# Optimization experiments

Hardware: AMD Instinct MI355X
Metric: run time of the kernel (lower is better)

## Reference

```python
import jax, jax.numpy as jnp
import numpy as np

B, S, D, H, E, K = 4, 2048, 1024, 2048, 8, 2


def setup_inputs() -> dict:
    key = jax.random.key(0)
    ks = jax.random.split(key, 5)
    x = jax.random.normal(ks[0], (B, S, D), dtype=jnp.float32)
    Wr = jax.random.normal(ks[1], (D, E), dtype=jnp.float32) * 0.02  # router weight
    w1 = jax.random.normal(ks[2], (E, D, H), dtype=jnp.float32) * 0.02  # gate proj per expert
    w3 = jax.random.normal(ks[3], (E, D, H), dtype=jnp.float32) * 0.02  # up proj per expert
    w2 = jax.random.normal(ks[4], (E, H, D), dtype=jnp.float32) * 0.02  # down proj per expert
    return {"x": x, "Wr": Wr, "w1": w1, "w2": w2, "w3": w3}


def reference(x, Wr, w1, w2, w3):
    b, s, d = x.shape
    e = Wr.shape[1]
    flat = x.reshape(b * s, d)                      # [T, D]
    logits = flat @ Wr                              # [T, E]
    probs = jax.nn.softmax(logits, axis=-1)
    vals, idx = jax.lax.top_k(probs, K)             # [T, K]
    weights = vals / jnp.sum(vals, axis=-1, keepdims=True)
    onehot = jax.nn.one_hot(idx, e, dtype=flat.dtype)   # [T, K, E]
    cw = jnp.einsum('tke,tk->te', onehot, weights)      # combine weight per (token, expert)

    # naive dense: every expert computes every token, masked by combine weights
    out = jnp.zeros_like(flat)
    for ei in range(e):  # fixed small structural loop over experts
        h = jax.nn.silu(flat @ w1[ei]) * (flat @ w3[ei])   # [T, H]
        out = out + (h @ w2[ei]) * cw[:, ei:ei + 1]

    # aux load-balancing loss (usage uses any() over top-k slots, as in torch code)
    usage = (onehot.sum(axis=1) > 0).astype(flat.dtype).mean(axis=0)  # [E]
    prob_mass = probs.mean(axis=0)                                     # [E]
    aux_loss = e * jnp.sum(usage * prob_mass)
    return out.reshape(b, s, d), aux_loss
```

## Files before the change

kernel.cpp:

```cpp
#include <hip/hip_runtime.h>
#include <hip/hip_bf16.h>
#include <cstdint>
#include <cstddef>

#define T_TOK 8192
#define DIM   1024
#define HID   2048
#define NE    8
#define CAP   2816

typedef __attribute__((ext_vector_type(8))) short bf16x8;
typedef __attribute__((ext_vector_type(4))) float f32x4;
using bf16 = __hip_bfloat16;

__device__ __forceinline__ void gload16(const bf16* g, bf16* l) {
    __builtin_amdgcn_global_load_lds(
        (const __attribute__((address_space(1))) unsigned int*)(g),
        (__attribute__((address_space(3))) unsigned int*)(l), 16, 0, 0);
}
__device__ __forceinline__ float b2f(unsigned short u) {
    return __uint_as_float(((unsigned int)u) << 16);
}
#define MFMA16(a, b, c) __builtin_amdgcn_mfma_f32_16x16x32_bf16((a), (b), (c), 0, 0, 0)
#define BARRIER() asm volatile("s_barrier" ::: "memory")
#define WAITVM6() asm volatile("s_waitcnt vmcnt(6)" ::: "memory")
#define WAITVM4() asm volatile("s_waitcnt vmcnt(4)" ::: "memory")
#define WAITVM0() asm volatile("s_waitcnt vmcnt(0)" ::: "memory")

__global__ __launch_bounds__(256) void k_transpose_all(const float* __restrict__ w1,
                                                       const float* __restrict__ w3,
                                                       const float* __restrict__ w2,
                                                       bf16* __restrict__ w1t,
                                                       bf16* __restrict__ w3t,
                                                       bf16* __restrict__ w2t) {
    __shared__ float tile[64][65];
    int z = blockIdx.z;
    const float* in = (z == 0) ? w1 : (z == 1) ? w3 : w2;
    bf16* out = (z == 0) ? w1t : (z == 1) ? w3t : w2t;
    int R = (z == 2) ? HID : DIM;
    int C = (z == 2) ? DIM : HID;
    int e = blockIdx.y;
    int ct = C >> 6;
    int r0 = (blockIdx.x / ct) << 6;
    int c0 = (blockIdx.x % ct) << 6;
    const float* src = in + (size_t)e * R * C;
    bf16* dst = out + (size_t)e * R * C;
    int s = threadIdx.x & 15, g = threadIdx.x >> 4;
#pragma unroll
    for (int j = 0; j < 4; ++j) {
        int row = j * 16 + g;
        float4 v = *(const float4*)(src + (size_t)(r0 + row) * C + c0 + s * 4);
        tile[row][s * 4 + 0] = v.x; tile[row][s * 4 + 1] = v.y;
        tile[row][s * 4 + 2] = v.z; tile[row][s * 4 + 3] = v.w;
    }
    __syncthreads();
#pragma unroll
    for (int j = 0; j < 4; ++j) {
        int c = j * 16 + g;
        int r = s * 4;
        bf16 o[4] = {__float2bfloat16(tile[r][c]),     __float2bfloat16(tile[r + 1][c]),
                     __float2bfloat16(tile[r + 2][c]), __float2bfloat16(tile[r + 3][c])};
        *(uint2*)(dst + (size_t)(c0 + c) * R + r0 + r) = *(const uint2*)o;
    }
}

__global__ __launch_bounds__(256) void k_logits(const float* __restrict__ x,
                                                const float* __restrict__ Wr,
                                                float* __restrict__ logits,
                                                bf16* __restrict__ xb) {
    __shared__ float wl[NE][DIM];
    for (int o = threadIdx.x; o < NE * DIM; o += 256) {
        int e = o >> 10, d = o & (DIM - 1);
        wl[e][d] = Wr[d * NE + e];
    }
    __syncthreads();
    int wid = threadIdx.x >> 6, lane = threadIdx.x & 63;
    int t = blockIdx.x * 4 + wid;
    const float* xr = x + (size_t)t * DIM;
    double acc[NE];
#pragma unroll
    for (int e = 0; e < NE; ++e) acc[e] = 0.0;
#pragma unroll
    for (int i = 0; i < DIM / 256; ++i) {
        int base = i * 256 + lane * 4;
        float4 v = *(const float4*)(xr + base);
        bf16 o[4] = {__float2bfloat16(v.x), __float2bfloat16(v.y),
                     __float2bfloat16(v.z), __float2bfloat16(v.w)};
        *(uint2*)(xb + (size_t)t * DIM + base) = *(const uint2*)o;
#pragma unroll
        for (int e = 0; e < NE; ++e)
            acc[e] += (double)v.x * wl[e][base] + (double)v.y * wl[e][base + 1]
                    + (double)v.z * wl[e][base + 2] + (double)v.w * wl[e][base + 3];
    }
#pragma unroll
    for (int e = 0; e < NE; ++e) {
        double v = acc[e];
        for (int m = 32; m >= 1; m >>= 1) v += __shfl_xor(v, m);
        if (lane == 0) logits[t * NE + e] = (float)v;
    }
}

__global__ __launch_bounds__(256) void k_route(const float* __restrict__ logits,
                                               int* counts, int* seg_tok, float* seg_w,
                                               int* slotpos, float* probsum) {
    int t = blockIdx.x * 256 + threadIdx.x;
    float l[NE];
#pragma unroll
    for (int e = 0; e < NE; ++e) l[e] = logits[t * NE + e];
    float mx = l[0];
#pragma unroll
    for (int e = 1; e < NE; ++e) mx = fmaxf(mx, l[e]);
    float p[NE], s = 0.f;
#pragma unroll
    for (int e = 0; e < NE; ++e) { p[e] = expf(l[e] - mx); s += p[e]; }
    float inv = 1.f / s;
#pragma unroll
    for (int e = 0; e < NE; ++e) p[e] *= inv;
    int e0 = 0; float v0 = p[0];
#pragma unroll
    for (int e = 1; e < NE; ++e) if (p[e] > v0) { v0 = p[e]; e0 = e; }
    int e1 = -1; float v1 = -1.f;
#pragma unroll
    for (int e = 0; e < NE; ++e) if (e != e0 && p[e] > v1) { v1 = p[e]; e1 = e; }
    float wsum = v0 + v1;
    float w0 = v0 / wsum, w1 = v1 / wsum;

    int lane = threadIdx.x & 63, wid = threadIdx.x >> 6;
    __shared__ float ps[4][NE];
#pragma unroll
    for (int e = 0; e < NE; ++e) {
        float v = p[e];
        for (int m = 32; m >= 1; m >>= 1) v += __shfl_xor(v, m);
        if (lane == 0) ps[wid][e] = v;
    }
    __syncthreads();
    if (threadIdx.x < NE) {
        float v = ps[0][threadIdx.x] + ps[1][threadIdx.x] + ps[2][threadIdx.x] + ps[3][threadIdx.x];
        atomicAdd(&probsum[threadIdx.x], v);
    }
    for (int slot = 0; slot < 2; ++slot) {
        int   e  = slot ? e1 : e0;
        float wv = slot ? w1 : w0;
#pragma unroll
        for (int ex = 0; ex < NE; ++ex) {
            unsigned long long m = __ballot(e == ex);
            if (e == ex) {
                int leader = __ffsll(m) - 1;
                int base = 0;
                if (lane == leader) base = atomicAdd(&counts[ex], __popcll(m));
                base = __shfl(base, leader);
                int pos = base + (int)__popcll(m & ((1ull << lane) - 1ull));
                if (pos < CAP) {
                    seg_tok[ex * CAP + pos] = t;
                    seg_w[ex * CAP + pos]  = wv;
                    slotpos[2 * t + slot]  = ex * CAP + pos;
                } else {
                    slotpos[2 * t + slot]  = -1;
                }
            }
        }
    }
}

__global__ __launch_bounds__(512, 2) void k_gemm1(const bf16* __restrict__ xb,
                                                  const bf16* __restrict__ w1t,
                                                  const bf16* __restrict__ w3t,
                                                  const int* __restrict__ counts,
                                                  const int* __restrict__ seg_tok,
                                                  bf16* __restrict__ h) {
    __shared__ __align__(16) bf16 lds[65536];
    __shared__ int toks[256];
    const int NTL = HID / 128;
    int flat = blockIdx.y * gridDim.x + blockIdx.x;
    int cpx  = (gridDim.x * NE) >> 3;
    int swz  = (flat & 7) * cpx + (flat >> 3);
    int e    = swz / gridDim.x;
    int tile = swz % gridDim.x;
    int mtile = tile / NTL, ntile = tile % NTL;
    int cnt = counts[e]; if (cnt > CAP) cnt = CAP;
    if (mtile * 256 >= cnt) return;

    int tx = threadIdx.x, lane = tx & 63, wid = tx >> 6;
    for (int i = tx; i < 256; i += 512) {
        int slot = mtile * 256 + i;
        toks[i] = seg_tok[e * CAP + (slot < cnt ? slot : 0)];
    }
    __syncthreads();

    int sr  = tx >> 2;
    int sc8 = (((tx & 3) ^ ((tx >> 3) & 3)) << 3);
    const bf16* sApLo = xb + (size_t)toks[sr]       * DIM + sc8;
    const bf16* sApHi = xb + (size_t)toks[128 + sr] * DIM + sc8;
    const bf16* sBg   = w1t + ((size_t)e * HID + ntile * 128 + sr) * DIM + sc8;
    const bf16* sBu   = w3t + ((size_t)e * HID + ntile * 128 + sr) * DIM + sc8;
    bf16* dA = lds + tx * 8;
    bf16* dB = lds + 32768 + tx * 8;

    int l15 = lane & 15, lh = lane >> 4;
    int wm = wid >> 2, wn = wid & 3;
    int ach = ((lh ^ ((l15 >> 1) & 3)) << 3);
    const bf16* rA = lds + (wm * 128 + l15) * 32 + ach;
    const bf16* rB = lds + 32768 + (wn * 32 + l15) * 32 + ach;

    f32x4 accg[8][2], accu[8][2];
    f32x4 zero4 = {0.f, 0.f, 0.f, 0.f};
#pragma unroll
    for (int m = 0; m < 8; ++m)
#pragma unroll
        for (int n = 0; n < 2; ++n) { accg[m][n] = zero4; accu[m][n] = zero4; }

#define STAGE_A1(s, ko) do { \
        gload16(sApLo + (ko), dA + (s) * 8192); \
        gload16(sApHi + (ko), dA + (s) * 8192 + 4096); } while (0)
#define STAGE_B1(s, ko) do { \
        gload16(sBg + (ko), dB + (s) * 8192); \
        gload16(sBu + (ko), dB + (s) * 8192 + 4096); } while (0)

    STAGE_A1(0, 0);  STAGE_B1(0, 0);
    STAGE_A1(1, 32); STAGE_B1(1, 32);

    const int NT = DIM / 32;
    bf16x8 g0, g1, u0, u1;
#pragma unroll 1
    for (int k = 0; k < NT; ++k) {
        int cs = (k & 3) * 8192, ps = (k + 2) & 3;
        bool st = (k + 2 < NT);
        int ko = (k + 2) * 32;
        if (st) STAGE_A1(ps, ko);
        if (k < NT - 2) WAITVM6(); else if (k < NT - 1) WAITVM4(); else WAITVM0();
        BARRIER();
        {
            const bf16* Ab = rA + cs;
            bf16x8 a0 = *(const bf16x8*)(Ab);
            bf16x8 a1 = *(const bf16x8*)(Ab + 512);
            bf16x8 a2 = *(const bf16x8*)(Ab + 1024);
            bf16x8 a3 = *(const bf16x8*)(Ab + 1536);
            const bf16* Bb = rB + cs;
            g0 = *(const bf16x8*)(Bb);
            g1 = *(const bf16x8*)(Bb + 512);
            u0 = *(const bf16x8*)(Bb + 4096);
            u1 = *(const bf16x8*)(Bb + 4608);
            __builtin_amdgcn_s_setprio(1);
            accg[0][0] = MFMA16(a0, g0, accg[0][0]); accg[1][0] = MFMA16(a1, g0, accg[1][0]);
            accg[2][0] = MFMA16(a2, g0, accg[2][0]); accg[3][0] = MFMA16(a3, g0, accg[3][0]);
            accg[0][1] = MFMA16(a0, g1, accg[0][1]); accg[1][1] = MFMA16(a1, g1, accg[1][1]);
            accg[2][1] = MFMA16(a2, g1, accg[2][1]); accg[3][1] = MFMA16(a3, g1, accg[3][1]);
            accu[0][0] = MFMA16(a0, u0, accu[0][0]); accu[1][0] = MFMA16(a1, u0, accu[1][0]);
            accu[2][0] = MFMA16(a2, u0, accu[2][0]); accu[3][0] = MFMA16(a3, u0, accu[3][0]);
            accu[0][1] = MFMA16(a0, u1, accu[0][1]); accu[1][1] = MFMA16(a1, u1, accu[1][1]);
            accu[2][1] = MFMA16(a2, u1, accu[2][1]); accu[3][1] = MFMA16(a3, u1, accu[3][1]);
            __builtin_amdgcn_s_setprio(0);
        }
        if (st) STAGE_B1(ps, ko);
        BARRIER();
        {
            const bf16* Ab = rA + cs + 2048;
            bf16x8 a4 = *(const bf16x8*)(Ab);
            bf16x8 a5 = *(const bf16x8*)(Ab + 512);
            bf16x8 a6 = *(const bf16x8*)(Ab + 1024);
            bf16x8 a7 = *(const bf16x8*)(Ab + 1536);
            __builtin_amdgcn_s_setprio(1);
            accg[4][0] = MFMA16(a4, g0, accg[4][0]); accg[5][0] = MFMA16(a5, g0, accg[5][0]);
            accg[6][0] = MFMA16(a6, g0, accg[6][0]); accg[7][0] = MFMA16(a7, g0, accg[7][0]);
            accg[4][1] = MFMA16(a4, g1, accg[4][1]); accg[5][1] = MFMA16(a5, g1, accg[5][1]);
            accg[6][1] = MFMA16(a6, g1, accg[6][1]); accg[7][1] = MFMA16(a7, g1, accg[7][1]);
            accu[4][0] = MFMA16(a4, u0, accu[4][0]); accu[5][0] = MFMA16(a5, u0, accu[5][0]);
            accu[6][0] = MFMA16(a6, u0, accu[6][0]); accu[7][0] = MFMA16(a7, u0, accu[7][0]);
            accu[4][1] = MFMA16(a4, u1, accu[4][1]); accu[5][1] = MFMA16(a5, u1, accu[5][1]);
            accu[6][1] = MFMA16(a6, u1, accu[6][1]); accu[7][1] = MFMA16(a7, u1, accu[7][1]);
            __builtin_amdgcn_s_setprio(0);
        }
    }
#undef STAGE_A1
#undef STAGE_B1

    bf16* hdst = h + ((size_t)e * CAP + (size_t)mtile * 256) * HID + ntile * 128;
#pragma unroll
    for (int m = 0; m < 8; ++m)
#pragma unroll
        for (int n = 0; n < 2; ++n)
#pragma unroll
            for (int r = 0; r < 4; ++r) {
                int row = wm * 128 + m * 16 + lh * 4 + r;
                int col = wn * 32 + n * 16 + l15;
                float gg = accg[m][n][r], uu = accu[m][n][r];
                float hv = gg / (1.f + __expf(-gg)) * uu;
                hdst[(size_t)row * HID + col] = __float2bfloat16(hv);
            }
}

__global__ __launch_bounds__(512, 2) void k_gemm2(const bf16* __restrict__ h,
                                                  const bf16* __restrict__ w2t,
                                                  const int* __restrict__ counts,
                                                  const float* __restrict__ seg_w,
                                                  bf16* __restrict__ ybuf) {
    __shared__ __align__(16) bf16 lds[65536];
    __shared__ float wts[256];
    const int NTL = DIM / 256;
    int flat = blockIdx.y * gridDim.x + blockIdx.x;
    int cpx  = (gridDim.x * NE) >> 3;
    int swz  = (flat & 7) * cpx + (flat >> 3);
    int e    = swz / gridDim.x;
    int tile = swz % gridDim.x;
    int mtile = tile / NTL, ntile = tile % NTL;
    int cnt = counts[e]; if (cnt > CAP) cnt = CAP;
    if (mtile * 256 >= cnt) return;

    int tx = threadIdx.x, lane = tx & 63, wid = tx >> 6;
    for (int i = tx; i < 256; i += 512) {
        int slot = mtile * 256 + i;
        wts[i] = (slot < cnt) ? seg_w[e * CAP + slot] : 0.f;
    }
    __syncthreads();

    int sr  = tx >> 2;
    int sc8 = (((tx & 3) ^ ((tx >> 3) & 3)) << 3);
    const bf16* sApLo = h + ((size_t)e * CAP + mtile * 256 + sr) * HID + sc8;
    const bf16* sApHi = h + ((size_t)e * CAP + mtile * 256 + 128 + sr) * HID + sc8;
    const bf16* sBpLo = w2t + ((size_t)e * DIM + ntile * 256 + sr) * HID + sc8;
    const bf16* sBpHi = w2t + ((size_t)e * DIM + ntile * 256 + 128 + sr) * HID + sc8;
    bf16* dA = lds + tx * 8;
    bf16* dB = lds + 32768 + tx * 8;

    int l15 = lane & 15, lh = lane >> 4;
    int wm = wid >> 2, wn = wid & 3;
    int ach = ((lh ^ ((l15 >> 1) & 3)) << 3);
    const bf16* rA = lds + (wm * 128 + l15) * 32 + ach;
    const bf16* rB = lds + 32768 + (wn * 64 + l15) * 32 + ach;

    f32x4 acc[8][4];
    f32x4 zero4 = {0.f, 0.f, 0.f, 0.f};
#pragma unroll
    for (int m = 0; m < 8; ++m)
#pragma unroll
        for (int n = 0; n < 4; ++n) acc[m][n] = zero4;

#define STAGE_A2(s, ko) do { \
        gload16(sApLo + (ko), dA + (s) * 8192); \
        gload16(sApHi + (ko), dA + (s) * 8192 + 4096); } while (0)
#define STAGE_B2(s, ko) do { \
        gload16(sBpLo + (ko), dB + (s) * 8192); \
        gload16(sBpHi + (ko), dB + (s) * 8192 + 4096); } while (0)

    STAGE_A2(0, 0);  STAGE_B2(0, 0);
    STAGE_A2(1, 32); STAGE_B2(1, 32);

    const int NT = HID / 32;
    bf16x8 b0, b1, b2, b3;
#pragma unroll 1
    for (int k = 0; k < NT; ++k) {
        int cs = (k & 3) * 8192, ps = (k + 2) & 3;
        bool st = (k + 2 < NT);
        int ko = (k + 2) * 32;
        if (st) STAGE_A2(ps, ko);
        if (k < NT - 2) WAITVM6(); else if (k < NT - 1) WAITVM4(); else WAITVM0();
        BARRIER();
        {
            const bf16* Ab = rA + cs;
            bf16x8 a0 = *(const bf16x8*)(Ab);
            bf16x8 a1 = *(const bf16x8*)(Ab + 512);
            bf16x8 a2 = *(const bf16x8*)(Ab + 1024);
            bf16x8 a3 = *(const bf16x8*)(Ab + 1536);
            const bf16* Bb = rB + cs;
            b0 = *(const bf16x8*)(Bb);
            b1 = *(const bf16x8*)(Bb + 512);
            b2 = *(const bf16x8*)(Bb + 1024);
            b3 = *(const bf16x8*)(Bb + 1536);
            __builtin_amdgcn_s_setprio(1);
            acc[0][0] = MFMA16(a0, b0, acc[0][0]); acc[1][0] = MFMA16(a1, b0, acc[1][0]);
            acc[2][0] = MFMA16(a2, b0, acc[2][0]); acc[3][0] = MFMA16(a3, b0, acc[3][0]);
            acc[0][1] = MFMA16(a0, b1, acc[0][1]); acc[1][1] = MFMA16(a1, b1, acc[1][1]);
            acc[2][1] = MFMA16(a2, b1, acc[2][1]); acc[3][1] = MFMA16(a3, b1, acc[3][1]);
            acc[0][2] = MFMA16(a0, b2, acc[0][2]); acc[1][2] = MFMA16(a1, b2, acc[1][2]);
            acc[2][2] = MFMA16(a2, b2, acc[2][2]); acc[3][2] = MFMA16(a3, b2, acc[3][2]);
            acc[0][3] = MFMA16(a0, b3, acc[0][3]); acc[1][3] = MFMA16(a1, b3, acc[1][3]);
            acc[2][3] = MFMA16(a2, b3, acc[2][3]); acc[3][3] = MFMA16(a3, b3, acc[3][3]);
            __builtin_amdgcn_s_setprio(0);
        }
        if (st) STAGE_B2(ps, ko);
        BARRIER();
        {
            const bf16* Ab = rA + cs + 2048;
            bf16x8 a4 = *(const bf16x8*)(Ab);
            bf16x8 a5 = *(const bf16x8*)(Ab + 512);
            bf16x8 a6 = *(const bf16x8*)(Ab + 1024);
            bf16x8 a7 = *(const bf16x8*)(Ab + 1536);
            __builtin_amdgcn_s_setprio(1);
            acc[4][0] = MFMA16(a4, b0, acc[4][0]); acc[5][0] = MFMA16(a5, b0, acc[5][0]);
            acc[6][0] = MFMA16(a6, b0, acc[6][0]); acc[7][0] = MFMA16(a7, b0, acc[7][0]);
            acc[4][1] = MFMA16(a4, b1, acc[4][1]); acc[5][1] = MFMA16(a5, b1, acc[5][1]);
            acc[6][1] = MFMA16(a6, b1, acc[6][1]); acc[7][1] = MFMA16(a7, b1, acc[7][1]);
            acc[4][2] = MFMA16(a4, b2, acc[4][2]); acc[5][2] = MFMA16(a5, b2, acc[5][2]);
            acc[6][2] = MFMA16(a6, b2, acc[6][2]); acc[7][2] = MFMA16(a7, b2, acc[7][2]);
            acc[4][3] = MFMA16(a4, b3, acc[4][3]); acc[5][3] = MFMA16(a5, b3, acc[5][3]);
            acc[6][3] = MFMA16(a6, b3, acc[6][3]); acc[7][3] = MFMA16(a7, b3, acc[7][3]);
            __builtin_amdgcn_s_setprio(0);
        }
    }
#undef STAGE_A2
#undef STAGE_B2

    bf16* ydst = ybuf + ((size_t)e * CAP + (size_t)mtile * 256) * DIM + ntile * 256;
#pragma unroll
    for (int m = 0; m < 8; ++m)
#pragma unroll
        for (int n = 0; n < 4; ++n)
#pragma unroll
            for (int r = 0; r < 4; ++r) {
                int row = wm * 128 + m * 16 + lh * 4 + r;
                int col = wn * 64 + n * 16 + l15;
                ydst[(size_t)row * DIM + col] = __float2bfloat16(acc[m][n][r] * wts[row]);
            }
}

__global__ __launch_bounds__(256) void k_combine(const bf16* __restrict__ yb,
                                                 const int* __restrict__ slotpos,
                                                 float* __restrict__ out) {
    int t = blockIdx.x;
    int s0 = slotpos[2 * t], s1 = slotpos[2 * t + 1];
    int d = threadIdx.x * 4;
    float4 a = {0.f, 0.f, 0.f, 0.f};
    if (s0 >= 0) {
        ushort4 v = *(const ushort4*)(yb + (size_t)s0 * DIM + d);
        a.x += b2f(v.x); a.y += b2f(v.y); a.z += b2f(v.z); a.w += b2f(v.w);
    }
    if (s1 >= 0) {
        ushort4 v = *(const ushort4*)(yb + (size_t)s1 * DIM + d);
        a.x += b2f(v.x); a.y += b2f(v.y); a.z += b2f(v.z); a.w += b2f(v.w);
    }
    *(float4*)(out + (size_t)t * DIM + d) = a;
}

__global__ void k_aux(const int* __restrict__ counts, const float* __restrict__ probsum,
                      float* __restrict__ outaux) {
    if (threadIdx.x == 0 && blockIdx.x == 0) {
        float s = 0.f;
        for (int e = 0; e < NE; ++e)
            s += ((float)counts[e] / (float)T_TOK) * (probsum[e] / (float)T_TOK);
        *outaux = (float)NE * s;
    }
}

extern "C" void kernel_launch(void* const* d_in, const int* in_sizes, int n_in,
                              void* d_out, int out_size, void* d_ws, size_t ws_size,
                              hipStream_t stream) {
    const float* x  = (const float*)d_in[0];
    const float* Wr = (const float*)d_in[1];
    const float* w1 = (const float*)d_in[2];
    const float* w2 = (const float*)d_in[3];
    const float* w3 = (const float*)d_in[4];
    float* out = (float*)d_out;

    char* ws = (char*)d_ws;
    size_t off = 0;
    auto alloc = [&](size_t bytes) { void* p = ws + off; off += (bytes + 255) & ~(size_t)255; return p; };
    bf16*  xb      = (bf16*)alloc((size_t)T_TOK * DIM * 2);
    bf16*  w1t     = (bf16*)alloc((size_t)NE * HID * DIM * 2);
    bf16*  w3t     = (bf16*)alloc((size_t)NE * HID * DIM * 2);
    bf16*  w2t     = (bf16*)alloc((size_t)NE * DIM * HID * 2);
    bf16*  hbuf    = (bf16*)alloc((size_t)NE * CAP * HID * 2);
    float* logits  = (float*)alloc((size_t)T_TOK * NE * 4);
    int*   counts  = (int*)alloc(256);
    int*   segtok  = (int*)alloc((size_t)NE * CAP * 4);
    float* segw    = (float*)alloc((size_t)NE * CAP * 4);
    int*   slotpos = (int*)alloc((size_t)T_TOK * 2 * 4);
    float* probsum = (float*)alloc(256);
    bf16*  ybuf    = w1t;
    (void)ws_size; (void)in_sizes; (void)n_in;

    hipMemsetAsync(counts, 0, 256, stream);
    hipMemsetAsync(probsum, 0, 256, stream);

    k_logits<<<T_TOK / 4, 256, 0, stream>>>(x, Wr, logits, xb);
    k_route<<<T_TOK / 256, 256, 0, stream>>>(logits, counts, segtok, segw, slotpos, probsum);

    dim3 gt((DIM / 64) * (HID / 64), NE, 3);
    k_transpose_all<<<gt, 256, 0, stream>>>(w1, w3, w2, w1t, w3t, w2t);

    dim3 g1((CAP / 256) * (HID / 128), NE);
    k_gemm1<<<g1, 512, 0, stream>>>(xb, w1t, w3t, counts, segtok, hbuf);
    dim3 g2((CAP / 256) * (DIM / 256), NE);
    k_gemm2<<<g2, 512, 0, stream>>>(hbuf, w2t, counts, segw, ybuf);

    k_combine<<<T_TOK, 256, 0, stream>>>(ybuf, slotpos, out);
    k_aux<<<1, 64, 0, stream>>>(counts, probsum, out + (size_t)T_TOK * DIM);
}
```

Measured before the change: 471.9 us.

## Deepen GEMM prefetch to three stages with a single barrier-split compute phase

```diff
diff --git a/kernel.cpp b/kernel.cpp
--- a/kernel.cpp
+++ b/kernel.cpp
@@ -9,6 +9,8 @@
 #define NE    8
 #define CAP   2816
 
+#define SLOTSZ 16384
+
 typedef __attribute__((ext_vector_type(8))) short bf16x8;
 typedef __attribute__((ext_vector_type(4))) float f32x4;
 using bf16 = __hip_bfloat16;
@@ -22,10 +24,17 @@
     return __uint_as_float(((unsigned int)u) << 16);
 }
 #define MFMA16(a, b, c) __builtin_amdgcn_mfma_f32_16x16x32_bf16((a), (b), (c), 0, 0, 0)
-#define BARRIER() asm volatile("s_barrier" ::: "memory")
-#define WAITVM6() asm volatile("s_waitcnt vmcnt(6)" ::: "memory")
-#define WAITVM4() asm volatile("s_waitcnt vmcnt(4)" ::: "memory")
-#define WAITVM0() asm volatile("s_waitcnt vmcnt(0)" ::: "memory")
+#define BARRIER()  asm volatile("s_barrier" ::: "memory")
+#define WAITVM12() asm volatile("s_waitcnt vmcnt(12)" ::: "memory")
+#define WAITVM8()  asm volatile("s_waitcnt vmcnt(8)" ::: "memory")
+#define WAITVM4()  asm volatile("s_waitcnt vmcnt(4)" ::: "memory")
+#define WAITVM0()  asm volatile("s_waitcnt vmcnt(0)" ::: "memory")
+#define VMGATE(k, NT) do { \
+        int rem_ = (NT) - 1 - (k); \
+        if (rem_ >= 3) WAITVM12(); \
+        else if (rem_ == 2) WAITVM8(); \
+        else if (rem_ == 1) WAITVM4(); \
+        else WAITVM0(); } while (0)
 
 __global__ __launch_bounds__(256) void k_transpose_all(const float* __restrict__ w1,
                                                        const float* __restrict__ w3,
@@ -162,13 +171,13 @@
     }
 }
 
-__global__ __launch_bounds__(512, 2) void k_gemm1(const bf16* __restrict__ xb,
+__global__ __launch_bounds__(512, 1) void k_gemm1(const bf16* __restrict__ xb,
                                                   const bf16* __restrict__ w1t,
                                                   const bf16* __restrict__ w3t,
                                                   const int* __restrict__ counts,
                                                   const int* __restrict__ seg_tok,
                                                   bf16* __restrict__ h) {
-    __shared__ __align__(16) bf16 lds[65536];
+    __shared__ __align__(16) bf16 lds[4 * SLOTSZ];
     __shared__ int toks[256];
     const int NTL = HID / 128;
     int flat = blockIdx.y * gridDim.x + blockIdx.x;
@@ -187,20 +196,18 @@
     }
     __syncthreads();
 
-    int sr  = tx >> 2;
-    int sc8 = (((tx & 3) ^ ((tx >> 3) & 3)) << 3);
-    const bf16* sApLo = xb + (size_t)toks[sr]       * DIM + sc8;
-    const bf16* sApHi = xb + (size_t)toks[128 + sr] * DIM + sc8;
-    const bf16* sBg   = w1t + ((size_t)e * HID + ntile * 128 + sr) * DIM + sc8;
-    const bf16* sBu   = w3t + ((size_t)e * HID + ntile * 128 + sr) * DIM + sc8;
-    bf16* dA = lds + tx * 8;
-    bf16* dB = lds + 32768 + tx * 8;
+    int srow = tx >> 2;
+    int sc8  = (((tx & 3) ^ ((tx >> 3) & 3)) << 3);
+    const bf16* sA0 = xb + (size_t)toks[srow]       * DIM + sc8;
+    const bf16* sA1 = xb + (size_t)toks[128 + srow] * DIM + sc8;
+    const bf16* sBg = w1t + ((size_t)e * HID + ntile * 128 + srow) * DIM + sc8;
+    const bf16* sBu = w3t + ((size_t)e * HID + ntile * 128 + srow) * DIM + sc8;
 
     int l15 = lane & 15, lh = lane >> 4;
     int wm = wid >> 2, wn = wid & 3;
     int ach = ((lh ^ ((l15 >> 1) & 3)) << 3);
-    const bf16* rA = lds + (wm * 128 + l15) * 32 + ach;
-    const bf16* rB = lds + 32768 + (wn * 32 + l15) * 32 + ach;
+    const int rAoff = (wm * 128 + l15) * 32 + ach;
+    const int rBoff = 8192 + (wn * 32 + l15) * 32 + ach;
 
     f32x4 accg[8][2], accu[8][2];
     f32x4 zero4 = {0.f, 0.f, 0.f, 0.f};
@@ -209,70 +216,54 @@
 #pragma unroll
         for (int n = 0; n < 2; ++n) { accg[m][n] = zero4; accu[m][n] = zero4; }
 
-#define STAGE_A1(s, ko) do { \
-        gload16(sApLo + (ko), dA + (s) * 8192); \
-        gload16(sApHi + (ko), dA + (s) * 8192 + 4096); } while (0)
-#define STAGE_B1(s, ko) do { \
-        gload16(sBg + (ko), dB + (s) * 8192); \
-        gload16(sBu + (ko), dB + (s) * 8192 + 4096); } while (0)
-
-    STAGE_A1(0, 0);  STAGE_B1(0, 0);
-    STAGE_A1(1, 32); STAGE_B1(1, 32);
-
+#define G1_STAGE(s, ko) do { \
+        bf16* d_ = lds + (s) * SLOTSZ + tx * 8; \
+        gload16(sA0 + (ko), d_); \
+        gload16(sA1 + (ko), d_ + 4096); \
+        gload16(sBg + (ko), d_ + 8192); \
+        gload16(sBu + (ko), d_ + 12288); } while (0)
+
+    G1_STAGE(0, 0); G1_STAGE(1, 32); G1_STAGE(2, 64);
     const int NT = DIM / 32;
-    bf16x8 g0, g1, u0, u1;
 #pragma unroll 1
     for (int k = 0; k < NT; ++k) {
-        int cs = (k & 3) * 8192, ps = (k + 2) & 3;
-        bool st = (k + 2 < NT);
-        int ko = (k + 2) * 32;
-        if (st) STAGE_A1(ps, ko);
-        if (k < NT - 2) WAITVM6(); else if (k < NT - 1) WAITVM4(); else WAITVM0();
+        if (k + 3 < NT) G1_STAGE((k + 3) & 3, (k + 3) * 32);
+        VMGATE(k, NT);
         BARRIER();
-        {
-            const bf16* Ab = rA + cs;
-            bf16x8 a0 = *(const bf16x8*)(Ab);
-            bf16x8 a1 = *(const bf16x8*)(Ab + 512);
-            bf16x8 a2 = *(const bf16x8*)(Ab + 1024);
-            bf16x8 a3 = *(const bf16x8*)(Ab + 1536);
-            const bf16* Bb = rB + cs;
-            g0 = *(const bf16x8*)(Bb);
-            g1 = *(const bf16x8*)(Bb + 512);
-            u0 = *(const bf16x8*)(Bb + 4096);
-            u1 = *(const bf16x8*)(Bb + 4608);
-            __builtin_amdgcn_s_setprio(1);
-            accg[0][0] = MFMA16(a0, g0, accg[0][0]); accg[1][0] = MFMA16(a1, g0, accg[1][0]);
-            accg[2][0] = MFMA16(a2, g0, accg[2][0]); accg[3][0] = MFMA16(a3, g0, accg[3][0]);
-            accg[0][1] = MFMA16(a0, g1, accg[0][1]); accg[1][1] = MFMA16(a1, g1, accg[1][1]);
-            accg[2][1] = MFMA16(a2, g1, accg[2][1]); accg[3][1] = MFMA16(a3, g1, accg[3][1]);
-            accu[0][0] = MFMA16(a0, u0, accu[0][0]); accu[1][0] = MFMA16(a1, u0, accu[1][0]);
-            accu[2][0] = MFMA16(a2, u0, accu[2][0]); accu[3][0] = MFMA16(a3, u0, accu[3][0]);
-            accu[0][1] = MFMA16(a0, u1, accu[0][1]); accu[1][1] = MFMA16(a1, u1, accu[1][1]);
-            accu[2][1] = MFMA16(a2, u1, accu[2][1]); accu[3][1] = MFMA16(a3, u1, accu[3][1]);
-            __builtin_amdgcn_s_setprio(0);
-        }
-        if (st) STAGE_B1(ps, ko);
+        const bf16* base = lds + (k & 3) * SLOTSZ;
+        bf16x8 a0 = *(const bf16x8*)(base + rAoff);
+        bf16x8 a1 = *(const bf16x8*)(base + rAoff + 512);
+        bf16x8 a2 = *(const bf16x8*)(base + rAoff + 1024);
+        bf16x8 a3 = *(const bf16x8*)(base + rAoff + 1536);
+        bf16x8 a4 = *(const bf16x8*)(base + rAoff + 2048);
+        bf16x8 a5 = *(const bf16x8*)(base + rAoff + 2560);
+        bf16x8 a6 = *(const bf16x8*)(base + rAoff + 3072);
+        bf16x8 a7 = *(const bf16x8*)(base + rAoff + 3584);
+        bf16x8 g0 = *(const bf16x8*)(base + rBoff);
+        bf16x8 g1 = *(const bf16x8*)(base + rBoff + 512);
+        bf16x8 u0 = *(const bf16x8*)(base + rBoff + 4096);
+        bf16x8 u1 = *(const bf16x8*)(base + rBoff + 4608);
+        __builtin_amdgcn_s_setprio(1);
+        accg[0][0] = MFMA16(a0, g0, accg[0][0]); accg[1][0] = MFMA16(a1, g0, accg[1][0]);
+        accg[2][0] = MFMA16(a2, g0, accg[2][0]); accg[3][0] = MFMA16(a3, g0, accg[3][0]);
+        accg[4][0] = MFMA16(a4, g0, accg[4][0]); accg[5][0] = MFMA16(a5, g0, accg[5][0]);
+        accg[6][0] = MFMA16(a6, g0, accg[6][0]); accg[7][0] = MFMA16(a7, g0, accg[7][0]);
+        accg[0][1] = MFMA16(a0, g1, accg[0][1]); accg[1][1] = MFMA16(a1, g1, accg[1][1]);
+        accg[2][1] = MFMA16(a2, g1, accg[2][1]); accg[3][1] = MFMA16(a3, g1, accg[3][1]);
+        accg[4][1] = MFMA16(a4, g1, accg[4][1]); accg[5][1] = MFMA16(a5, g1, accg[5][1]);
+        accg[6][1] = MFMA16(a6, g1, accg[6][1]); accg[7][1] = MFMA16(a7, g1, accg[7][1]);
+        accu[0][0] = MFMA16(a0, u0, accu[0][0]); accu[1][0] = MFMA16(a1, u0, accu[1][0]);
+        accu[2][0] = MFMA16(a2, u0, accu[2][0]); accu[3][0] = MFMA16(a3, u0, accu[3][0]);
+        accu[4][0] = MFMA16(a4, u0, accu[4][0]); accu[5][0] = MFMA16(a5, u0, accu[5][0]);
+        accu[6][0] = MFMA16(a6, u0, accu[6][0]); accu[7][0] = MFMA16(a7, u0, accu[7][0]);
+        accu[0][1] = MFMA16(a0, u1, accu[0][1]); accu[1][1] = MFMA16(a1, u1, accu[1][1]);
+        accu[2][1] = MFMA16(a2, u1, accu[2][1]); accu[3][1] = MFMA16(a3, u1, accu[3][1]);
+        accu[4][1] = MFMA16(a4, u1, accu[4][1]); accu[5][1] = MFMA16(a5, u1, accu[5][1]);
+        accu[6][1] = MFMA16(a6, u1, accu[6][1]); accu[7][1] = MFMA16(a7, u1, accu[7][1]);
+        __builtin_amdgcn_s_setprio(0);
         BARRIER();
-        {
-            const bf16* Ab = rA + cs + 2048;
-            bf16x8 a4 = *(const bf16x8*)(Ab);
-            bf16x8 a5 = *(const bf16x8*)(Ab + 512);
-            bf16x8 a6 = *(const bf16x8*)(Ab + 1024);
-            bf16x8 a7 = *(const bf16x8*)(Ab + 1536);
-            __builtin_amdgcn_s_setprio(1);
-            accg[4][0] = MFMA16(a4, g0, accg[4][0]); accg[5][0] = MFMA16(a5, g0, accg[5][0]);
-            accg[6][0] = MFMA16(a6, g0, accg[6][0]); accg[7][0] = MFMA16(a7, g0, accg[7][0]);
-            accg[4][1] = MFMA16(a4, g1, accg[4][1]); accg[5][1] = MFMA16(a5, g1, accg[5][1]);
-            accg[6][1] = MFMA16(a6, g1, accg[6][1]); accg[7][1] = MFMA16(a7, g1, accg[7][1]);
-            accu[4][0] = MFMA16(a4, u0, accu[4][0]); accu[5][0] = MFMA16(a5, u0, accu[5][0]);
-            accu[6][0] = MFMA16(a6, u0, accu[6][0]); accu[7][0] = MFMA16(a7, u0, accu[7][0]);
-            accu[4][1] = MFMA16(a4, u1, accu[4][1]); accu[5][1] = MFMA16(a5, u1, accu[5][1]);
-            accu[6][1] = MFMA16(a6, u1, accu[6][1]); accu[7][1] = MFMA16(a7, u1, accu[7][1]);
-            __builtin_amdgcn_s_setprio(0);
-        }
-    }
-#undef STAGE_A1
-#undef STAGE_B1
+    }
+#undef G1_STAGE
 
     bf16* hdst = h + ((size_t)e * CAP + (size_t)mtile * 256) * HID + ntile * 128;
 #pragma unroll
@@ -289,12 +280,12 @@
             }
 }
 
-__global__ __launch_bounds__(512, 2) void k_gemm2(const bf16* __restrict__ h,
+__global__ __launch_bounds__(512, 1) void k_gemm2(const bf16* __restrict__ hbuf,
                                                   const bf16* __restrict__ w2t,
                                                   const int* __restrict__ counts,
                                                   const float* __restrict__ seg_w,
                                                   bf16* __restrict__ ybuf) {
-    __shared__ __align__(16) bf16 lds[65536];
+    __shared__ __align__(16) bf16 lds[4 * SLOTSZ];
     __shared__ float wts[256];
     const int NTL = DIM / 256;
     int flat = blockIdx.y * gridDim.x + blockIdx.x;
@@ -313,20 +304,18 @@
     }
     __syncthreads();
 
-    int sr  = tx >> 2;
-    int sc8 = (((tx & 3) ^ ((tx >> 3) & 3)) << 3);
-    const bf16* sApLo = h + ((size_t)e * CAP + mtile * 256 + sr) * HID + sc8;
-    const bf16* sApHi = h + ((size_t)e * CAP + mtile * 256 + 128 + sr) * HID + sc8;
-    const bf16* sBpLo = w2t + ((size_t)e * DIM + ntile * 256 + sr) * HID + sc8;
-    const bf16* sBpHi = w2t + ((size_t)e * DIM + ntile * 256 + 128 + sr) * HID + sc8;
-    bf16* dA = lds + tx * 8;
-    bf16* dB = lds + 32768 + tx * 8;
+    int srow = tx >> 2;
+    int sc8  = (((tx & 3) ^ ((tx >> 3) & 3)) << 3);
+    const bf16* sA0 = hbuf + ((size_t)e * CAP + mtile * 256 + srow) * HID + sc8;
+    const bf16* sA1 = hbuf + ((size_t)e * CAP + mtile * 256 + 128 + srow) * HID + sc8;
+    const bf16* sB0 = w2t + ((size_t)e * DIM + ntile * 256 + srow) * HID + sc8;
+    const bf16* sB1 = w2t + ((size_t)e * DIM + ntile * 256 + 128 + srow) * HID + sc8;
 
     int l15 = lane & 15, lh = lane >> 4;
     int wm = wid >> 2, wn = wid & 3;
     int ach = ((lh ^ ((l15 >> 1) & 3)) << 3);
-    const bf16* rA = lds + (wm * 128 + l15) * 32 + ach;
-    const bf16* rB = lds + 32768 + (wn * 64 + l15) * 32 + ach;
+    const int rAoff = (wm * 128 + l15) * 32 + ach;
+    const int rBoff = 8192 + (wn * 64 + l15) * 32 + ach;
 
     f32x4 acc[8][4];
     f32x4 zero4 = {0.f, 0.f, 0.f, 0.f};
@@ -335,70 +324,54 @@
 #pragma unroll
         for (int n = 0; n < 4; ++n) acc[m][n] = zero4;
 
-#define STAGE_A2(s, ko) do { \
-        gload16(sApLo + (ko), dA + (s) * 8192); \
-        gload16(sApHi + (ko), dA + (s) * 8192 + 4096); } while (0)
-#define STAGE_B2(s, ko) do { \
-        gload16(sBpLo + (ko), dB + (s) * 8192); \
-        gload16(sBpHi + (ko), dB + (s) * 8192 + 4096); } while (0)
-
-    STAGE_A2(0, 0);  STAGE_B2(0, 0);
-    STAGE_A2(1, 32); STAGE_B2(1, 32);
-
+#define G2_STAGE(s, ko) do { \
+        bf16* d_ = lds + (s) * SLOTSZ + tx * 8; \
+        gload16(sA0 + (ko), d_); \
+        gload16(sA1 + (ko), d_ + 4096); \
+        gload16(sB0 + (ko), d_ + 8192); \
+        gload16(sB1 + (ko), d_ + 12288); } while (0)
+
+    G2_STAGE(0, 0); G2_STAGE(1, 32); G2_STAGE(2, 64);
     const int NT = HID / 32;
-    bf16x8 b0, b1, b2, b3;
 #pragma unroll 1
     for (int k = 0; k < NT; ++k) {
-        int cs = (k & 3) * 8192, ps = (k + 2) & 3;
-        bool st = (k + 2 < NT);
-        int ko = (k + 2) * 32;
-        if (st) STAGE_A2(ps, ko);
-        if (k < NT - 2) WAITVM6(); else if (k < NT - 1) WAITVM4(); else WAITVM0();
+        if (k + 3 < NT) G2_STAGE((k + 3) & 3, (k + 3) * 32);
+        VMGATE(k, NT);
         BARRIER();
-        {
-            const bf16* Ab = rA + cs;
-            bf16x8 a0 = *(const bf16x8*)(Ab);
-            bf16x8 a1 = *(const bf16x8*)(Ab + 512);
-            bf16x8 a2 = *(const bf16x8*)(Ab + 1024);
-            bf16x8 a3 = *(const bf16x8*)(Ab + 1536);
-            const bf16* Bb = rB + cs;
-            b0 = *(const bf16x8*)(Bb);
-            b1 = *(const bf16x8*)(Bb + 512);
-            b2 = *(const bf16x8*)(Bb + 1024);
-            b3 = *(const bf16x8*)(Bb + 1536);
-            __builtin_amdgcn_s_setprio(1);
-            acc[0][0] = MFMA16(a0, b0, acc[0][0]); acc[1][0] = MFMA16(a1, b0, acc[1][0]);
-            acc[2][0] = MFMA16(a2, b0, acc[2][0]); acc[3][0] = MFMA16(a3, b0, acc[3][0]);
-            acc[0][1] = MFMA16(a0, b1, acc[0][1]); acc[1][1] = MFMA16(a1, b1, acc[1][1]);
-            acc[2][1] = MFMA16(a2, b1, acc[2][1]); acc[3][1] = MFMA16(a3, b1, acc[3][1]);
-            acc[0][2] = MFMA16(a0, b2, acc[0][2]); acc[1][2] = MFMA16(a1, b2, acc[1][2]);
-            acc[2][2] = MFMA16(a2, b2, acc[2][2]); acc[3][2] = MFMA16(a3, b2, acc[3][2]);
-            acc[0][3] = MFMA16(a0, b3, acc[0][3]); acc[1][3] = MFMA16(a1, b3, acc[1][3]);
-            acc[2][3] = MFMA16(a2, b3, acc[2][3]); acc[3][3] = MFMA16(a3, b3, acc[3][3]);
-            __builtin_amdgcn_s_setprio(0);
-        }
-        if (st) STAGE_B2(ps, ko);
+        const bf16* base = lds + (k & 3) * SLOTSZ;
+        bf16x8 a0 = *(const bf16x8*)(base + rAoff);
+        bf16x8 a1 = *(const bf16x8*)(base + rAoff + 512);
+        bf16x8 a2 = *(const bf16x8*)(base + rAoff + 1024);
+        bf16x8 a3 = *(const bf16x8*)(base + rAoff + 1536);
+        bf16x8 a4 = *(const bf16x8*)(base + rAoff + 2048);
+        bf16x8 a5 = *(const bf16x8*)(base + rAoff + 2560);
+        bf16x8 a6 = *(const bf16x8*)(base + rAoff + 3072);
+        bf16x8 a7 = *(const bf16x8*)(base + rAoff + 3584);
+        bf16x8 b0 = *(const bf16x8*)(base + rBoff);
+        bf16x8 b1 = *(const bf16x8*)(base + rBoff + 512);
+        bf16x8 b2 = *(const bf16x8*)(base + rBoff + 1024);
+        bf16x8 b3 = *(const bf16x8*)(base + rBoff + 1536);
+        __builtin_amdgcn_s_setprio(1);
+        acc[0][0] = MFMA16(a0, b0, acc[0][0]); acc[1][0] = MFMA16(a1, b0, acc[1][0]);
+        acc[2][0] = MFMA16(a2, b0, acc[2][0]); acc[3][0] = MFMA16(a3, b0, acc[3][0]);
+        acc[4][0] = MFMA16(a4, b0, acc[4][0]); acc[5][0] = MFMA16(a5, b0, acc[5][0]);
+        acc[6][0] = MFMA16(a6, b0, acc[6][0]); acc[7][0] = MFMA16(a7, b0, acc[7][0]);
+        acc[0][1] = MFMA16(a0, b1, acc[0][1]); acc[1][1] = MFMA16(a1, b1, acc[1][1]);
+        acc[2][1] = MFMA16(a2, b1, acc[2][1]); acc[3][1] = MFMA16(a3, b1, acc[3][1]);
+        acc[4][1] = MFMA16(a4, b1, acc[4][1]); acc[5][1] = MFMA16(a5, b1, acc[5][1]);
+        acc[6][1] = MFMA16(a6, b1, acc[6][1]); acc[7][1] = MFMA16(a7, b1, acc[7][1]);
+        acc[0][2] = MFMA16(a0, b2, acc[0][2]); acc[1][2] = MFMA16(a1, b2, acc[1][2]);
+        acc[2][2] = MFMA16(a2, b2, acc[2][2]); acc[3][2] = MFMA16(a3, b2, acc[3][2]);
+        acc[4][2] = MFMA16(a4, b2, acc[4][2]); acc[5][2] = MFMA16(a5, b2, acc[5][2]);
+        acc[6][2] = MFMA16(a6, b2, acc[6][2]); acc[7][2] = MFMA16(a7, b2, acc[7][2]);
+        acc[0][3] = MFMA16(a0, b3, acc[0][3]); acc[1][3] = MFMA16(a1, b3, acc[1][3]);
+        acc[2][3] = MFMA16(a2, b3, acc[2][3]); acc[3][3] = MFMA16(a3, b3, acc[3][3]);
+        acc[4][3] = MFMA16(a4, b3, acc[4][3]); acc[5][3] = MFMA16(a5, b3, acc[5][3]);
+        acc[6][3] = MFMA16(a6, b3, acc[6][3]); acc[7][3] = MFMA16(a7, b3, acc[7][3]);
+        __builtin_amdgcn_s_setprio(0);
         BARRIER();
-        {
-            const bf16* Ab = rA + cs + 2048;
-            bf16x8 a4 = *(const bf16x8*)(Ab);
-            bf16x8 a5 = *(const bf16x8*)(Ab + 512);
-            bf16x8 a6 = *(const bf16x8*)(Ab + 1024);
-            bf16x8 a7 = *(const bf16x8*)(Ab + 1536);
-            __builtin_amdgcn_s_setprio(1);
-            acc[4][0] = MFMA16(a4, b0, acc[4][0]); acc[5][0] = MFMA16(a5, b0, acc[5][0]);
-            acc[6][0] = MFMA16(a6, b0, acc[6][0]); acc[7][0] = MFMA16(a7, b0, acc[7][0]);
-            acc[4][1] = MFMA16(a4, b1, acc[4][1]); acc[5][1] = MFMA16(a5, b1, acc[5][1]);
-            acc[6][1] = MFMA16(a6, b1, acc[6][1]); acc[7][1] = MFMA16(a7, b1, acc[7][1]);
-            acc[4][2] = MFMA16(a4, b2, acc[4][2]); acc[5][2] = MFMA16(a5, b2, acc[5][2]);
-            acc[6][2] = MFMA16(a6, b2, acc[6][2]); acc[7][2] = MFMA16(a7, b2, acc[7][2]);
-            acc[4][3] = MFMA16(a4, b3, acc[4][3]); acc[5][3] = MFMA16(a5, b3, acc[5][3]);
-            acc[6][3] = MFMA16(a6, b3, acc[6][3]); acc[7][3] = MFMA16(a7, b3, acc[7][3]);
-            __builtin_amdgcn_s_setprio(0);
-        }
-    }
-#undef STAGE_A2
-#undef STAGE_B2
+    }
+#undef G2_STAGE
 
     bf16* ydst = ybuf + ((size_t)e * CAP + (size_t)mtile * 256) * DIM + ntile * 256;
 #pragma unroll
```

Result: slower. 505.0 us (+7.0%).
